# Kernel tuning notes

Measured on AMD Instinct MI355X. Metric: run time of the kernel, lower is better.

## Reference

```python
import jax, jax.numpy as jnp
import numpy as np

N = 50000      # nodes
E = 800000     # edges (before self-loops)
IN = 128       # in_channels
HID = 32       # hidden_channels
HEADS = 4
OUT = 2        # out_channels
NEG_SLOPE = 0.2  # PyG GATConv default LeakyReLU slope


def gat_layer(x, src, dst, W, a_src, a_dst, b, n_nodes, concat):
    """PyG GATConv (eval mode, self-loops already appended to src/dst).
    x: [N, in], W: [in, H*F], a_src/a_dst: [H, F], b: [H*F] or [F].
    """
    H, F = a_src.shape
    h = (x @ W).reshape(n_nodes, H, F)              # [N, H, F]
    al_s = (h * a_src).sum(-1)                      # [N, H] per-node src logit
    al_d = (h * a_dst).sum(-1)                      # [N, H] per-node dst logit
    e = al_s[src] + al_d[dst]                       # [E', H]
    e = jnp.where(e > 0, e, NEG_SLOPE * e)          # LeakyReLU
    # segment softmax over edges grouped by destination node
    m = jax.ops.segment_max(e, dst, num_segments=n_nodes)
    m = jnp.where(jnp.isfinite(m), m, 0.0)
    num = jnp.exp(e - m[dst])                       # [E', H]
    den = jax.ops.segment_sum(num, dst, num_segments=n_nodes)
    alpha = num / (den[dst] + 1e-16)                # [E', H]
    out = jax.ops.segment_sum(alpha[:, :, None] * h[src], dst, num_segments=n_nodes)  # [N, H, F]
    out = out.reshape(n_nodes, H * F) if concat else out.mean(axis=1)
    return out + b


def setup_inputs() -> dict:
    key = jax.random.key(0)
    ks = jax.random.split(key, 16)
    HID4 = HID // 4
    inp = {
        "x": jax.random.normal(ks[0], (N, IN), dtype=jnp.float32),
        "edge_index": jax.random.randint(ks[1], (2, E), 0, N, dtype=jnp.int64),
        "edge_attr": jax.random.normal(ks[2], (E, 8), dtype=jnp.float32),
        # conv1: in=IN -> HID per head, HEADS heads, concat
        "W1": jax.random.normal(ks[3], (IN, HEADS * HID), dtype=jnp.float32) * (1.0 / np.sqrt(IN)),
        "a_src1": jax.random.normal(ks[4], (HEADS, HID), dtype=jnp.float32) * 0.1,
        "a_dst1": jax.random.normal(ks[5], (HEADS, HID), dtype=jnp.float32) * 0.1,
        "b1": jnp.zeros((HEADS * HID,), dtype=jnp.float32),
        # conv2: in=HEADS*HID -> HID//4, 1 head, mean (concat=False)
        "W2": jax.random.normal(ks[6], (HEADS * HID, HID4), dtype=jnp.float32) * (1.0 / np.sqrt(HEADS * HID)),
        "a_src2": jax.random.normal(ks[7], (1, HID4), dtype=jnp.float32) * 0.1,
        "a_dst2": jax.random.normal(ks[8], (1, HID4), dtype=jnp.float32) * 0.1,
        "b2": jnp.zeros((HID4,), dtype=jnp.float32),
        # final linear
        "Wl": jax.random.normal(ks[9], (HID4, OUT), dtype=jnp.float32) * (1.0 / np.sqrt(HID4)),
        "bl": jnp.zeros((OUT,), dtype=jnp.float32),
    }
    return inp


def reference(x, edge_index, edge_attr, W1, a_src1, a_dst1, b1,
              W2, a_src2, a_dst2, b2, Wl, bl):
    # edge_attr is ignored (GATConv built without edge_dim). Eval mode: dropout is identity.
    loop = jnp.arange(N, dtype=edge_index.dtype)
    src = jnp.concatenate([edge_index[0], loop])  # PyG adds self-loops by default
    dst = jnp.concatenate([edge_index[1], loop])
    h = jax.nn.elu(gat_layer(x, src, dst, W1, a_src1, a_dst1, b1, N, concat=True))
    h = jax.nn.elu(gat_layer(h, src, dst, W2, a_src2, a_dst2, b2, N, concat=False))
    return jax.nn.sigmoid(h @ Wl + bl)
```

## Files before the change

### kernel.cpp

```cpp
#include <hip/hip_runtime.h>
#include <math.h>

#define TPB 256
#define GN 64
#define CAP 64
#define LOG2E 1.44269504088896f

typedef short bf16x8 __attribute__((ext_vector_type(8)));
typedef float floatx4 __attribute__((ext_vector_type(4)));

__device__ __forceinline__ float elu_f(float x)  { return x > 0.f ? x : __expf(x) - 1.f; }
__device__ __forceinline__ float sigmoid_f(float x){ return 1.f / (1.f + __expf(-x)); }
__device__ __forceinline__ float leaky(float x)  { return fmaxf(x, 0.2f * x); }

__device__ __forceinline__ unsigned short f2bf(float f) {
    unsigned int u = __float_as_uint(f);
    return (unsigned short)((u + 0x7FFFu + ((u >> 16) & 1u)) >> 16);
}
__device__ __forceinline__ float bf_lo(unsigned int u) { return __uint_as_float(u << 16); }
__device__ __forceinline__ float bf_hi(unsigned int u) { return __uint_as_float(u & 0xffff0000u); }

static inline int cdiv(long long a, int b) { return (int)((a + b - 1) / b); }

__global__ __launch_bounds__(256) void gemm1_mfma(
        const float* __restrict__ x, const float* __restrict__ W,
        const float* __restrict__ a_src, const float* __restrict__ a_dst,
        unsigned short* __restrict__ hb, float* __restrict__ als, float* __restrict__ ald,
        int* __restrict__ cursor, int N) {
    __shared__ unsigned short xs[GN][136];
    __shared__ unsigned short wt[128][136];
    int tid = threadIdx.x;
    int n0 = blockIdx.x * GN;
    if (tid < GN) { int i = n0 + tid; if (i < N) cursor[i] = 0; }

#pragma unroll
    for (int i = 0; i < 8; i++) {
        int idx = tid + i * 256;
        int r = idx >> 5;
        int c4 = (idx & 31) * 4;
        int row = n0 + r; if (row >= N) row = N - 1;
        float4 v = *(const float4*)(x + (size_t)row * 128 + c4);
        unsigned short* p = &xs[r][c4];
        p[0] = f2bf(v.x); p[1] = f2bf(v.y); p[2] = f2bf(v.z); p[3] = f2bf(v.w);
    }
#pragma unroll
    for (int i = 0; i < 16; i++) {
        int idx = tid + i * 256;
        int k = idx >> 5;
        int c4 = (idx & 31) * 4;
        float4 v = *(const float4*)(W + (size_t)k * 128 + c4);
        wt[c4 + 0][k] = f2bf(v.x);
        wt[c4 + 1][k] = f2bf(v.y);
        wt[c4 + 2][k] = f2bf(v.z);
        wt[c4 + 3][k] = f2bf(v.w);
    }
    __syncthreads();

    int w = tid >> 6;
    int lane = tid & 63;
    int idx16 = lane & 15, quad = lane >> 4;
    int nw = n0 + w * 16;

    bf16x8 af[4];
#pragma unroll
    for (int kc = 0; kc < 4; kc++)
        af[kc] = *(const bf16x8*)(&xs[w * 16 + idx16][kc * 32 + quad * 8]);

    floatx4 accs[8];
#pragma unroll
    for (int cg = 0; cg < 8; cg++) {
        floatx4 acc = {0.f, 0.f, 0.f, 0.f};
#pragma unroll
        for (int kc = 0; kc < 4; kc++) {
            bf16x8 bf = *(const bf16x8*)(&wt[cg * 16 + idx16][kc * 32 + quad * 8]);
            acc = __builtin_amdgcn_mfma_f32_16x16x32_bf16(af[kc], bf, acc, 0, 0, 0);
        }
        accs[cg] = acc;
    }

    float asr[8], adr[8];
#pragma unroll
    for (int cg = 0; cg < 8; cg++) {
        asr[cg] = a_src[cg * 16 + idx16];
        adr[cg] = a_dst[cg * 16 + idx16];
    }
    float ps[16], pd[16];
#pragma unroll
    for (int i = 0; i < 16; i++) { ps[i] = 0.f; pd[i] = 0.f; }
#pragma unroll
    for (int cg = 0; cg < 8; cg++) {
        int h = cg >> 1;
#pragma unroll
        for (int r = 0; r < 4; r++) {
            ps[r * 4 + h] = fmaf(accs[cg][r], asr[cg], ps[r * 4 + h]);
            pd[r * 4 + h] = fmaf(accs[cg][r], adr[cg], pd[r * 4 + h]);
        }
    }
#pragma unroll
    for (int i = 0; i < 16; i++) {
        ps[i] += __shfl_xor(ps[i], 1); ps[i] += __shfl_xor(ps[i], 2);
        ps[i] += __shfl_xor(ps[i], 4); ps[i] += __shfl_xor(ps[i], 8);
        pd[i] += __shfl_xor(pd[i], 1); pd[i] += __shfl_xor(pd[i], 2);
        pd[i] += __shfl_xor(pd[i], 4); pd[i] += __shfl_xor(pd[i], 8);
    }
    float myps = 0.f, mypd = 0.f;
#pragma unroll
    for (int i = 0; i < 16; i++) {
        if (i == idx16) { myps = ps[i]; mypd = pd[i]; }
    }
    int rowl = nw + quad * 4 + (idx16 >> 2);
    if (rowl < N) {
        als[rowl * 4 + (idx16 & 3)] = myps * LOG2E;
        ald[rowl * 4 + (idx16 & 3)] = mypd * LOG2E;
    }
#pragma unroll
    for (int cg = 0; cg < 8; cg++) {
#pragma unroll
        for (int r = 0; r < 4; r++) {
            int row = nw + quad * 4 + r;
            if (row < N) hb[(size_t)row * 128 + cg * 16 + idx16] = f2bf(accs[cg][r]);
        }
    }
}

__global__ void scatter_kernel(const int* __restrict__ ei, int E, float invg,
                               int* __restrict__ cursor, unsigned short* __restrict__ slots) {
    int myg = blockIdx.x & 7;
    int p = (blockIdx.x >> 3) * blockDim.x + threadIdx.x;
    int e0 = p * 2;
    if (e0 >= E) return;
    int d0 = ei[E + e0];
    if ((int)((float)d0 * invg) == myg) {
        int s = ei[e0];
        int pos = atomicAdd(&cursor[d0], 1);
        if (pos < CAP) slots[((size_t)d0 << 6) + pos] = (unsigned short)s;
    }
    int e1 = e0 + 1;
    if (e1 < E) {
        int d1 = ei[E + e1];
        if ((int)((float)d1 * invg) == myg) {
            int s = ei[e1];
            int pos = atomicAdd(&cursor[d1], 1);
            if (pos < CAP) slots[((size_t)d1 << 6) + pos] = (unsigned short)s;
        }
    }
}

__global__ void accum1_fused(const int* __restrict__ cursor, const unsigned short* __restrict__ slots,
                             const unsigned short* __restrict__ hb,
                             const float* __restrict__ als, const float* __restrict__ ald,
                             const float* __restrict__ b, const float* __restrict__ W2,
                             const float* __restrict__ a_src2, const float* __restrict__ a_dst2,
                             float* __restrict__ h2, float* __restrict__ als2,
                             float* __restrict__ ald2, int N) {
    int t = blockIdx.x * blockDim.x + threadIdx.x;
    int n = t >> 6;
    if (n >= N) return;
    int lane = t & 63;
    int eslot = lane >> 4;
    int fg = lane & 15;
    int hd = fg >> 2;

    float ald_h = ald[n * 4 + hd];
    int cnt = cursor[n];
    const unsigned short* cp = slots + ((size_t)n << 6);

    float acc[8];
#pragma unroll
    for (int k = 0; k < 8; k++) acc[k] = 0.f;
    float den = 0.f;
    if (eslot == 0) {
        float wself = exp2f(leaky(als[n * 4 + hd] + ald_h));
        uint4 us = *(const uint4*)(hb + (size_t)n * 128 + fg * 8);
        acc[0] = wself * bf_lo(us.x); acc[1] = wself * bf_hi(us.x);
        acc[2] = wself * bf_lo(us.y); acc[3] = wself * bf_hi(us.y);
        acc[4] = wself * bf_lo(us.z); acc[5] = wself * bf_hi(us.z);
        acc[6] = wself * bf_lo(us.w); acc[7] = wself * bf_hi(us.w);
        den = wself;
    }

    if (cnt > 0) {
        int i0 = eslot < cnt ? eslot : cnt - 1;
        int s_c = cp[i0];
        float al_c = als[s_c * 4 + hd];
        uint4 u_c = *(const uint4*)(hb + (size_t)s_c * 128 + fg * 8);
        for (int base = 0; base < cnt; base += 4) {
            int nxt = base + 4 + eslot;
            int ic = nxt < cnt ? nxt : cnt - 1;
            int s_n = cp[ic];
            float al_n = als[s_n * 4 + hd];
            uint4 u_n = *(const uint4*)(hb + (size_t)s_n * 128 + fg * 8);

            float w = exp2f(leaky(al_c + ald_h));
            if (base + eslot >= cnt) w = 0.f;
            acc[0] = fmaf(w, bf_lo(u_c.x), acc[0]);
            acc[1] = fmaf(w, bf_hi(u_c.x), acc[1]);
            acc[2] = fmaf(w, bf_lo(u_c.y), acc[2]);
            acc[3] = fmaf(w, bf_hi(u_c.y), acc[3]);
            acc[4] = fmaf(w, bf_lo(u_c.z), acc[4]);
            acc[5] = fmaf(w, bf_hi(u_c.z), acc[5]);
            acc[6] = fmaf(w, bf_lo(u_c.w), acc[6]);
            acc[7] = fmaf(w, bf_hi(u_c.w), acc[7]);
            den += w;

            al_c = al_n; u_c = u_n;
        }
    }

#pragma unroll
    for (int k = 0; k < 8; k++) {
        acc[k] += __shfl_xor(acc[k], 16);
        acc[k] += __shfl_xor(acc[k], 32);
    }
    den += __shfl_xor(den, 16);
    den += __shfl_xor(den, 32);

    float inv = 1.f / (den + 1e-16f);
    float bv[8];
    *(float4*)(bv)     = *(const float4*)(b + fg * 8);
    *(float4*)(bv + 4) = *(const float4*)(b + fg * 8 + 4);
    float o[8];
#pragma unroll
    for (int k = 0; k < 8; k++) o[k] = elu_f(acc[k] * inv + bv[k]);

    int srcl = lane >> 2;
    float tmp[8];
#pragma unroll
    for (int k = 0; k < 8; k++) tmp[k] = __shfl(o[k], srcl);
    int sel = lane & 3;
    float o0 = sel == 0 ? tmp[0] : sel == 1 ? tmp[2] : sel == 2 ? tmp[4] : tmp[6];
    float o1 = sel == 0 ? tmp[1] : sel == 1 ? tmp[3] : sel == 2 ? tmp[5] : tmp[7];

    float w2a[8], w2b[8];
#pragma unroll
    for (int c = 0; c < 8; c += 4) {
        *(float4*)(w2a + c) = *(const float4*)(W2 + (size_t)(2 * lane) * 8 + c);
        *(float4*)(w2b + c) = *(const float4*)(W2 + (size_t)(2 * lane + 1) * 8 + c);
    }
    float part[8];
#pragma unroll
    for (int c = 0; c < 8; c++)
        part[c] = fmaf(o0, w2a[c], o1 * w2b[c]);
#pragma unroll
    for (int c = 0; c < 8; c++) {
        part[c] += __shfl_xor(part[c], 1);
        part[c] += __shfl_xor(part[c], 2);
        part[c] += __shfl_xor(part[c], 4);
    }
    int ch = lane & 7;
    float v = part[0];
    v = ch == 1 ? part[1] : v;  v = ch == 2 ? part[2] : v;  v = ch == 3 ? part[3] : v;
    v = ch == 4 ? part[4] : v;  v = ch == 5 ? part[5] : v;  v = ch == 6 ? part[6] : v;
    v = ch == 7 ? part[7] : v;
    v += __shfl_xor(v, 8); v += __shfl_xor(v, 16); v += __shfl_xor(v, 32);
    if (lane < 8) h2[(size_t)n * 8 + lane] = v;
    float ps = v * a_src2[ch];
    float pd = v * a_dst2[ch];
    ps += __shfl_xor(ps, 1); ps += __shfl_xor(ps, 2); ps += __shfl_xor(ps, 4);
    pd += __shfl_xor(pd, 1); pd += __shfl_xor(pd, 2); pd += __shfl_xor(pd, 4);
    if (lane == 0) {
        als2[n] = ps * LOG2E;
        ald2[n] = pd * LOG2E;
    }
}

__global__ void accum2_final(const int* __restrict__ cursor, const unsigned short* __restrict__ slots,
                             const float* __restrict__ h2,
                             const float* __restrict__ als, const float* __restrict__ ald,
                             const float* __restrict__ b2, const float* __restrict__ Wl,
                             const float* __restrict__ bl, float* __restrict__ out, int N) {
    int t = blockIdx.x * blockDim.x + threadIdx.x;
    int n = t >> 6;
    if (n >= N) return;
    int lane = t & 63;
    int slot = lane >> 3;
    int c = lane & 7;

    float ald_n = ald[n];
    int cnt = cursor[n];
    const unsigned short* cp = slots + ((size_t)n << 6);

    float den = 0.f, acc = 0.f;
    if (slot == 0) {
        float wself = exp2f(leaky(als[n] + ald_n));
        acc = wself * h2[(size_t)n * 8 + c];
        den = wself;
    }

    if (cnt > 0) {
        int i0 = slot < cnt ? slot : cnt - 1;
        int s_c = cp[i0];
        float al_c = als[s_c];
        float h_c = h2[(size_t)s_c * 8 + c];
        for (int base = 0; base < cnt; base += 8) {
            int nxt = base + 8 + slot;
            int ic = nxt < cnt ? nxt : cnt - 1;
            int s_n = cp[ic];
            float al_n = als[s_n];
            float h_n = h2[(size_t)s_n * 8 + c];

            float w = exp2f(leaky(al_c + ald_n));
            if (base + slot >= cnt) w = 0.f;
            acc = fmaf(w, h_c, acc);
            den += w;

            al_c = al_n; h_c = h_n;
        }
    }
    acc += __shfl_xor(acc, 8);  acc += __shfl_xor(acc, 16); acc += __shfl_xor(acc, 32);
    den += __shfl_xor(den, 8);  den += __shfl_xor(den, 16); den += __shfl_xor(den, 32);

    float inv = 1.f / (den + 1e-16f);
    float o = elu_f(acc * inv + b2[c]);
    float r0 = o * Wl[c * 2 + 0];
    float r1 = o * Wl[c * 2 + 1];
    r0 += __shfl_xor(r0, 1); r0 += __shfl_xor(r0, 2); r0 += __shfl_xor(r0, 4);
    r1 += __shfl_xor(r1, 1); r1 += __shfl_xor(r1, 2); r1 += __shfl_xor(r1, 4);
    if (lane == 0) {
        float2 r;
        r.x = sigmoid_f(r0 + bl[0]);
        r.y = sigmoid_f(r1 + bl[1]);
        *(float2*)(out + (size_t)n * 2) = r;
    }
}

extern "C" void kernel_launch(void* const* d_in, const int* in_sizes, int n_in,
                              void* d_out, int out_size, void* d_ws, size_t ws_size,
                              hipStream_t stream) {
    const float* x      = (const float*)d_in[0];
    const int*   ei     = (const int*)d_in[1];
    const float* W1     = (const float*)d_in[3];
    const float* a_src1 = (const float*)d_in[4];
    const float* a_dst1 = (const float*)d_in[5];
    const float* b1     = (const float*)d_in[6];
    const float* W2     = (const float*)d_in[7];
    const float* a_src2 = (const float*)d_in[8];
    const float* a_dst2 = (const float*)d_in[9];
    const float* b2     = (const float*)d_in[10];
    const float* Wl     = (const float*)d_in[11];
    const float* bl     = (const float*)d_in[12];
    float* out = (float*)d_out;

    const int N = in_sizes[0] / 128;
    const int E = in_sizes[1] / 2;
    const int gsz = cdiv(N, 8);
    const float invg = 1.f / (float)gsz;

    unsigned short* h1b = (unsigned short*)d_ws;
    float* als1 = (float*)d_ws + (size_t)N * 64;
    float* ald1 = als1 + (size_t)N * 4;
    float* h2   = ald1 + (size_t)N * 4;
    float* als2 = h2   + (size_t)N * 8;
    float* ald2 = als2 + (size_t)N;
    int* cursor = (int*)(ald2 + (size_t)N);
    unsigned short* slots = (unsigned short*)(cursor + N);
    (void)ws_size; (void)n_in; (void)out_size;

    gemm1_mfma<<<cdiv(N, GN), 256, 0, stream>>>(x, W1, a_src1, a_dst1, h1b, als1, ald1, cursor, N);
    scatter_kernel<<<8 * cdiv(cdiv(E, 2), TPB), TPB, 0, stream>>>(ei, E, invg, cursor, slots);
    accum1_fused<<<cdiv((long long)N * 64, TPB), TPB, 0, stream>>>(
        cursor, slots, h1b, als1, ald1, b1, W2, a_src2, a_dst2, h2, als2, ald2, N);
    accum2_final<<<cdiv((long long)N * 64, TPB), TPB, 0, stream>>>(
        cursor, slots, h2, als2, ald2, b2, Wl, bl, out, N);
}
```

Baseline: 235.7 us.

## Merge GEMM and edge scatter into one launch, store self-loop as slot zero

The edge-scatter work now runs as extra blocks of the GEMM kernel, so the dense projection and the atomic CSR build overlap within a single launch. A small init kernel, which must finish before the scatter starts, zeroes the cursors and puts each node's self-loop into slot 0. This lets both aggregation kernels drop their special self-loop branch and the cnt>0 guard. In exchange it adds one more launch, the GEMM blocks may occupy the device unevenly next to the scatter blocks, and the self-loop now uses one of the 64 slot entries.

```diff
diff --git a/kernel.cpp b/kernel.cpp
--- a/kernel.cpp
+++ b/kernel.cpp
@@ -22,17 +22,50 @@
 
 static inline int cdiv(long long a, int b) { return (int)((a + b - 1) / b); }
 
-__global__ __launch_bounds__(256) void gemm1_mfma(
+__global__ void init_kernel(int* __restrict__ cursor, unsigned short* __restrict__ slots, int N) {
+    int i = blockIdx.x * blockDim.x + threadIdx.x;
+    if (i < N) {
+        cursor[i] = 1;
+        slots[(size_t)i << 6] = (unsigned short)i;
+    }
+}
+
+__global__ __launch_bounds__(256) void gemm1_scatter(
         const float* __restrict__ x, const float* __restrict__ W,
         const float* __restrict__ a_src, const float* __restrict__ a_dst,
         unsigned short* __restrict__ hb, float* __restrict__ als, float* __restrict__ ald,
-        int* __restrict__ cursor, int N) {
+        const int* __restrict__ ei, int E, float invg,
+        int* __restrict__ cursor, unsigned short* __restrict__ slots,
+        int GB, int N) {
     __shared__ unsigned short xs[GN][136];
     __shared__ unsigned short wt[128][136];
     int tid = threadIdx.x;
+
+    if (blockIdx.x >= GB) {
+        int sb = blockIdx.x - GB;
+        int myg = sb & 7;
+        int p = (sb >> 3) * blockDim.x + tid;
+        int e0 = p * 2;
+        if (e0 >= E) return;
+        int d0 = ei[E + e0];
+        if ((int)((float)d0 * invg) == myg) {
+            int s = ei[e0];
+            int pos = atomicAdd(&cursor[d0], 1);
+            if (pos < CAP) slots[((size_t)d0 << 6) + pos] = (unsigned short)s;
+        }
+        int e1 = e0 + 1;
+        if (e1 < E) {
+            int d1 = ei[E + e1];
+            if ((int)((float)d1 * invg) == myg) {
+                int s = ei[e1];
+                int pos = atomicAdd(&cursor[d1], 1);
+                if (pos < CAP) slots[((size_t)d1 << 6) + pos] = (unsigned short)s;
+            }
+        }
+        return;
+    }
+
     int n0 = blockIdx.x * GN;
-    if (tid < GN) { int i = n0 + tid; if (i < N) cursor[i] = 0; }
-
 #pragma unroll
     for (int i = 0; i < 8; i++) {
         int idx = tid + i * 256;
@@ -40,8 +73,8 @@
         int c4 = (idx & 31) * 4;
         int row = n0 + r; if (row >= N) row = N - 1;
         float4 v = *(const float4*)(x + (size_t)row * 128 + c4);
-        unsigned short* p = &xs[r][c4];
-        p[0] = f2bf(v.x); p[1] = f2bf(v.y); p[2] = f2bf(v.z); p[3] = f2bf(v.w);
+        unsigned short* pp = &xs[r][c4];
+        pp[0] = f2bf(v.x); pp[1] = f2bf(v.y); pp[2] = f2bf(v.z); pp[3] = f2bf(v.w);
     }
 #pragma unroll
     for (int i = 0; i < 16; i++) {
@@ -119,29 +152,6 @@
         for (int r = 0; r < 4; r++) {
             int row = nw + quad * 4 + r;
             if (row < N) hb[(size_t)row * 128 + cg * 16 + idx16] = f2bf(accs[cg][r]);
-        }
-    }
-}
-
-__global__ void scatter_kernel(const int* __restrict__ ei, int E, float invg,
-                               int* __restrict__ cursor, unsigned short* __restrict__ slots) {
-    int myg = blockIdx.x & 7;
-    int p = (blockIdx.x >> 3) * blockDim.x + threadIdx.x;
-    int e0 = p * 2;
-    if (e0 >= E) return;
-    int d0 = ei[E + e0];
-    if ((int)((float)d0 * invg) == myg) {
-        int s = ei[e0];
-        int pos = atomicAdd(&cursor[d0], 1);
-        if (pos < CAP) slots[((size_t)d0 << 6) + pos] = (unsigned short)s;
-    }
-    int e1 = e0 + 1;
-    if (e1 < E) {
-        int d1 = ei[E + e1];
-        if ((int)((float)d1 * invg) == myg) {
-            int s = ei[e1];
-            int pos = atomicAdd(&cursor[d1], 1);
-            if (pos < CAP) slots[((size_t)d1 << 6) + pos] = (unsigned short)s;
         }
     }
 }
@@ -162,49 +172,39 @@
     int hd = fg >> 2;
 
     float ald_h = ald[n * 4 + hd];
-    int cnt = cursor[n];
+    int cnt = cursor[n]; if (cnt > CAP) cnt = CAP;
     const unsigned short* cp = slots + ((size_t)n << 6);
+
+    int i0 = eslot < cnt ? eslot : cnt - 1;
+    int s_c = cp[i0];
+    float al_c = als[s_c * 4 + hd];
+    uint4 u_c = *(const uint4*)(hb + (size_t)s_c * 128 + fg * 8);
 
     float acc[8];
 #pragma unroll
     for (int k = 0; k < 8; k++) acc[k] = 0.f;
     float den = 0.f;
-    if (eslot == 0) {
-        float wself = exp2f(leaky(als[n * 4 + hd] + ald_h));
-        uint4 us = *(const uint4*)(hb + (size_t)n * 128 + fg * 8);
-        acc[0] = wself * bf_lo(us.x); acc[1] = wself * bf_hi(us.x);
-        acc[2] = wself * bf_lo(us.y); acc[3] = wself * bf_hi(us.y);
-        acc[4] = wself * bf_lo(us.z); acc[5] = wself * bf_hi(us.z);
-        acc[6] = wself * bf_lo(us.w); acc[7] = wself * bf_hi(us.w);
-        den = wself;
-    }
-
-    if (cnt > 0) {
-        int i0 = eslot < cnt ? eslot : cnt - 1;
-        int s_c = cp[i0];
-        float al_c = als[s_c * 4 + hd];
-        uint4 u_c = *(const uint4*)(hb + (size_t)s_c * 128 + fg * 8);
-        for (int base = 0; base < cnt; base += 4) {
-            int nxt = base + 4 + eslot;
-            int ic = nxt < cnt ? nxt : cnt - 1;
-            int s_n = cp[ic];
-            float al_n = als[s_n * 4 + hd];
-            uint4 u_n = *(const uint4*)(hb + (size_t)s_n * 128 + fg * 8);
-
-            float w = exp2f(leaky(al_c + ald_h));
-            if (base + eslot >= cnt) w = 0.f;
-            acc[0] = fmaf(w, bf_lo(u_c.x), acc[0]);
-            acc[1] = fmaf(w, bf_hi(u_c.x), acc[1]);
-            acc[2] = fmaf(w, bf_lo(u_c.y), acc[2]);
-            acc[3] = fmaf(w, bf_hi(u_c.y), acc[3]);
-            acc[4] = fmaf(w, bf_lo(u_c.z), acc[4]);
-            acc[5] = fmaf(w, bf_hi(u_c.z), acc[5]);
-            acc[6] = fmaf(w, bf_lo(u_c.w), acc[6]);
-            acc[7] = fmaf(w, bf_hi(u_c.w), acc[7]);
-            den += w;
-
-            al_c = al_n; u_c = u_n;
-        }
+
+    for (int base = 0; base < cnt; base += 4) {
+        int nxt = base + 4 + eslot;
+        int ic = nxt < cnt ? nxt : cnt - 1;
+        int s_n = cp[ic];
+        float al_n = als[s_n * 4 + hd];
+        uint4 u_n = *(const uint4*)(hb + (size_t)s_n * 128 + fg * 8);
+
+        float w = exp2f(leaky(al_c + ald_h));
+        if (base + eslot >= cnt) w = 0.f;
+        acc[0] = fmaf(w, bf_lo(u_c.x), acc[0]);
+        acc[1] = fmaf(w, bf_hi(u_c.x), acc[1]);
+        acc[2] = fmaf(w, bf_lo(u_c.y), acc[2]);
+        acc[3] = fmaf(w, bf_hi(u_c.y), acc[3]);
+        acc[4] = fmaf(w, bf_lo(u_c.z), acc[4]);
+        acc[5] = fmaf(w, bf_hi(u_c.z), acc[5]);
+        acc[6] = fmaf(w, bf_lo(u_c.w), acc[6]);
+        acc[7] = fmaf(w, bf_hi(u_c.w), acc[7]);
+        den += w;
+
+        al_c = al_n; u_c = u_n;
     }
 
 #pragma unroll
@@ -254,13 +254,13 @@
     v = ch == 7 ? part[7] : v;
     v += __shfl_xor(v, 8); v += __shfl_xor(v, 16); v += __shfl_xor(v, 32);
     if (lane < 8) h2[(size_t)n * 8 + lane] = v;
-    float ps = v * a_src2[ch];
-    float pd = v * a_dst2[ch];
-    ps += __shfl_xor(ps, 1); ps += __shfl_xor(ps, 2); ps += __shfl_xor(ps, 4);
-    pd += __shfl_xor(pd, 1); pd += __shfl_xor(pd, 2); pd += __shfl_xor(pd, 4);
+    float ps2 = v * a_src2[ch];
+    float pd2 = v * a_dst2[ch];
+    ps2 += __shfl_xor(ps2, 1); ps2 += __shfl_xor(ps2, 2); ps2 += __shfl_xor(ps2, 4);
+    pd2 += __shfl_xor(pd2, 1); pd2 += __shfl_xor(pd2, 2); pd2 += __shfl_xor(pd2, 4);
     if (lane == 0) {
-        als2[n] = ps * LOG2E;
-        ald2[n] = pd * LOG2E;
+        als2[n] = ps2 * LOG2E;
+        ald2[n] = pd2 * LOG2E;
     }
 }
 
@@ -277,35 +277,28 @@
     int c = lane & 7;
 
     float ald_n = ald[n];
-    int cnt = cursor[n];
+    int cnt = cursor[n]; if (cnt > CAP) cnt = CAP;
     const unsigned short* cp = slots + ((size_t)n << 6);
 
+    int i0 = slot < cnt ? slot : cnt - 1;
+    int s_c = cp[i0];
+    float al_c = als[s_c];
+    float h_c = h2[(size_t)s_c * 8 + c];
+
     float den = 0.f, acc = 0.f;
-    if (slot == 0) {
-        float wself = exp2f(leaky(als[n] + ald_n));
-        acc = wself * h2[(size_t)n * 8 + c];
-        den = wself;
-    }
-
-    if (cnt > 0) {
-        int i0 = slot < cnt ? slot : cnt - 1;
-        int s_c = cp[i0];
-        float al_c = als[s_c];
-        float h_c = h2[(size_t)s_c * 8 + c];
-        for (int base = 0; base < cnt; base += 8) {
-            int nxt = base + 8 + slot;
-            int ic = nxt < cnt ? nxt : cnt - 1;
-            int s_n = cp[ic];
-            float al_n = als[s_n];
-            float h_n = h2[(size_t)s_n * 8 + c];
-
-            float w = exp2f(leaky(al_c + ald_n));
-            if (base + slot >= cnt) w = 0.f;
-            acc = fmaf(w, h_c, acc);
-            den += w;
-
-            al_c = al_n; h_c = h_n;
-        }
+    for (int base = 0; base < cnt; base += 8) {
+        int nxt = base + 8 + slot;
+        int ic = nxt < cnt ? nxt : cnt - 1;
+        int s_n = cp[ic];
+        float al_n = als[s_n];
+        float h_n = h2[(size_t)s_n * 8 + c];
+
+        float w = exp2f(leaky(al_c + ald_n));
+        if (base + slot >= cnt) w = 0.f;
+        acc = fmaf(w, h_c, acc);
+        den += w;
+
+        al_c = al_n; h_c = h_n;
     }
     acc += __shfl_xor(acc, 8);  acc += __shfl_xor(acc, 16); acc += __shfl_xor(acc, 32);
     den += __shfl_xor(den, 8);  den += __shfl_xor(den, 16); den += __shfl_xor(den, 32);
@@ -345,6 +338,8 @@
     const int E = in_sizes[1] / 2;
     const int gsz = cdiv(N, 8);
     const float invg = 1.f / (float)gsz;
+    const int GB = cdiv(N, GN);
+    const int SB = 8 * cdiv(cdiv(E, 2), TPB);
 
     unsigned short* h1b = (unsigned short*)d_ws;
     float* als1 = (float*)d_ws + (size_t)N * 64;
@@ -356,8 +351,9 @@
     unsigned short* slots = (unsigned short*)(cursor + N);
     (void)ws_size; (void)n_in; (void)out_size;
 
-    gemm1_mfma<<<cdiv(N, GN), 256, 0, stream>>>(x, W1, a_src1, a_dst1, h1b, als1, ald1, cursor, N);
-    scatter_kernel<<<8 * cdiv(cdiv(E, 2), TPB), TPB, 0, stream>>>(ei, E, invg, cursor, slots);
+    init_kernel<<<cdiv(N, TPB), TPB, 0, stream>>>(cursor, slots, N);
+    gemm1_scatter<<<GB + SB, 256, 0, stream>>>(x, W1, a_src1, a_dst1, h1b, als1, ald1,
+                                               ei, E, invg, cursor, slots, GB, N);
     accum1_fused<<<cdiv((long long)N * 64, TPB), TPB, 0, stream>>>(
         cursor, slots, h1b, als1, ald1, b1, W2, a_src2, a_dst2, h2, als2, ald2, N);
     accum2_final<<<cdiv((long long)N * 64, TPB), TPB, 0, stream>>>(
```

Measured after the change: 234.7 us. Within noise of the previous version (-0.4%).
